# Kernel optimization log

Hardware: AMD Instinct MI355X
Metric: run time of the kernel (lower is better)

The kernel has to match this reference:

```python
import jax, jax.numpy as jnp
import numpy as np

N = 4096        # nodes == batch_size (GFN operates on dense N x N adjacency)
E = 65536       # edges per view (avg degree 16)
IN = 512        # per-view input feature dim
HV = [128, 64]  # per-view GCN dims
HM = [64, 64]   # fused-graph GCN dims
VIEWS = 3


def setup_inputs() -> dict:
    key = jax.random.key(0)
    ks = iter(jax.random.split(key, 64))

    def xavier(shape):
        lim = float(np.sqrt(6.0 / (shape[0] + shape[1])))
        return jax.random.uniform(next(ks), shape, minval=-lim, maxval=lim, dtype=jnp.float32)

    inp = {}
    for v in range(VIEWS):
        inp[f"x{v}"] = jax.random.normal(next(ks), (N, IN), dtype=jnp.float32)
        inp[f"src{v}"] = jax.random.randint(next(ks), (E,), 0, N, dtype=jnp.int32)
        inp[f"dst{v}"] = jax.random.randint(next(ks), (E,), 0, N, dtype=jnp.int32)
        inp[f"Wv{v}0"] = xavier((IN, HV[0]))
        inp[f"bv{v}0"] = jnp.zeros((HV[0],), jnp.float32)
        inp[f"Wv{v}1"] = xavier((HV[0], HV[1]))
        inp[f"bv{v}1"] = jnp.zeros((HV[1],), jnp.float32)
        inp[f"Wf{v}"] = xavier((HV[1], HV[1]))  # FeatureFusion weight
    # GFN: Linear(N -> N/2) -> ReLU -> Linear(N/2 -> N)
    inp["Wg1"] = xavier((N, N // 2)); inp["bg1"] = jnp.zeros((N // 2,), jnp.float32)
    inp["Wg2"] = xavier((N // 2, N)); inp["bg2"] = jnp.zeros((N,), jnp.float32)
    # fused-graph GCN layers
    inp["Wm0"] = xavier((HV[1], HM[0])); inp["bm0"] = jnp.zeros((HM[0],), jnp.float32)
    inp["Wm1"] = xavier((HM[0], HM[1])); inp["bm1"] = jnp.zeros((HM[1],), jnp.float32)
    return inp


def _deg_norms(src, dst):
    # DGL GraphConv norm='both': scale by out-deg(src)^-1/2 and in-deg(dst)^-1/2, degrees clamped to >=1
    ones = jnp.ones(src.shape[0], jnp.float32)
    dout = jnp.maximum(jax.ops.segment_sum(ones, src, num_segments=N), 1.0)
    din = jnp.maximum(jax.ops.segment_sum(ones, dst, num_segments=N), 1.0)
    return dout ** -0.5, din ** -0.5


def _gconv(x, W, b, src, dst, do_isqrt, di_isqrt, act):
    h = (x * do_isqrt[:, None]) @ W            # [N, out] (W commutes with row scaling)
    agg = jax.ops.segment_sum(h[src], dst, num_segments=N)
    h = agg * di_isqrt[:, None] + b
    return act(h)


def reference(x0, x1, x2, src0, dst0, src1, dst1, src2, dst2,
              Wv00, bv00, Wv01, bv01, Wv10, bv10, Wv11, bv11, Wv20, bv20, Wv21, bv21,
              Wf0, Wf1, Wf2, Wg1, bg1, Wg2, bg2, Wm0, bm0, Wm1, bm1):
    ident = lambda t: t
    xs = [x0, x1, x2]
    edges = [(src0, dst0), (src1, dst1), (src2, dst2)]
    Wv = [(Wv00, bv00, Wv01, bv01), (Wv10, bv10, Wv11, bv11), (Wv20, bv20, Wv21, bv21)]
    Wf = [Wf0, Wf1, Wf2]

    # per-view GCN stacks (relu on first layer, identity on last)
    feats = []
    for v in range(VIEWS):
        src, dst = edges[v]
        do_i, di_i = _deg_norms(src, dst)
        W0, b0, W1, b1 = Wv[v]
        f = _gconv(xs[v], W0, b0, src, dst, do_i, di_i, jax.nn.relu)
        f = _gconv(f, W1, b1, src, dst, do_i, di_i, ident)
        feats.append(f)

    # FeatureFusion (dropout omitted for determinism): sum(f @ Wf), softmax over features, relu
    z = feats[0] @ Wf[0] + feats[1] @ Wf[1] + feats[2] @ Wf[2]
    z = jax.nn.relu(jax.nn.softmax(z, axis=1))

    # consensus graph: sum of per-view dense adjacencies -> GFN -> clamp -> round(+0.1)
    adj = jnp.zeros((N, N), jnp.float32)
    for src, dst in edges:
        adj = adj + jnp.zeros((N, N), jnp.float32).at[src, dst].set(1.0)
    fused = jax.nn.relu(adj @ Wg1 + bg1) @ Wg2 + bg2
    fused = jnp.round(jnp.clip(fused, 0.0, 1.0) + 0.1)
    adj_r = fused

    # rebuild binary graph (went through numpy in original -> stop_gradient), symmetrize, add self-loops
    sym = jax.lax.stop_gradient(fused)
    sym = sym + sym.T
    A = jnp.maximum((sym > 0).astype(jnp.float32), jnp.eye(N, dtype=jnp.float32))
    deg = A.sum(axis=1)
    dn = deg ** -0.5

    # fused-graph GCN layers (dense normalized SpMM form since A is already dense)
    h = z
    h = jax.nn.relu(((A @ (h * dn[:, None])) * dn[:, None]) @ Wm0 + bm0)
    h = ((A @ (h * dn[:, None])) * dn[:, None]) @ Wm1 + bm1

    # InnerProductDecoder with identity activation; all `views` entries of adj_rec are identical
    adj_rec = h @ h.T
    return (adj_r, adj_rec, h)
```

## Files before the change

### kernel.cpp

```cpp
#include <hip/hip_runtime.h>
#include <math.h>

#define NNODES 4096
#define NEDGES 65536

typedef short bf16x8 __attribute__((ext_vector_type(8)));
typedef short short4v __attribute__((ext_vector_type(4)));
typedef float f32x4 __attribute__((ext_vector_type(4)));

struct Ptr3  { const float* p[3]; };
struct Ptr3i { const int*   p[3]; };
struct Ptr3h { const short* p[3]; };

__device__ __forceinline__ short f2bf(float f) {
    unsigned u = __builtin_bit_cast(unsigned, f);
    unsigned r = (u + 0x7FFFu + ((u >> 16) & 1u)) >> 16;
    return (short)r;
}

__device__ __forceinline__ void gload_lds16(const void* g, void* l) {
    __builtin_amdgcn_global_load_lds(
        (const __attribute__((address_space(1))) unsigned*)g,
        (__attribute__((address_space(3))) unsigned*)l, 16, 0, 0);
}

template<int BN, int ACT>
__global__ __launch_bounds__(512, 1)
void g8_k(const short* __restrict__ A, const short* __restrict__ Bt,
          const float* __restrict__ bias, void* __restrict__ Cout,
          unsigned char* __restrict__ Pout, int M, int Nn, int K, int lda, int ldb)
{
    constexpr int SLOT_SH = 16384 + BN * 64;
    constexpr int WN = (BN == 256) ? 4 : 2;
    constexpr int TM = (BN == 256) ? 128 : 64;
    constexpr int MF = TM / 32;
    __shared__ short lds[2 * SLOT_SH];

    const int tid = threadIdx.x;
    const int lane = tid & 63;
    const int wave = tid >> 6;
    const int wm = wave / WN, wn = wave % WN;
    const int gx = gridDim.x, nwg = gx * gridDim.y;
    int w = blockIdx.y * gx + blockIdx.x;
    const int q8 = nwg >> 3;
    w = (w & 7) * q8 + (w >> 3);
    const int bm0 = (w / gx) * 256, bn0 = (w % gx) * BN;

    const int NT = K >> 6;

    f32x4 acc[2 * MF][4] = {};
    bf16x8 aF[MF][2];
    bf16x8 bF[2][2][2];

    auto stageQ = [&](int t, int sel) {
        if (sel < 0 || t >= NT) return;
        const int k0 = t << 6;
        short* L = lds + (t & 1) * SLOT_SH;
        const int rowq = tid >> 3;
        const int slot8 = tid & 7;
        const int woff = wave * 512;
#pragma unroll
        for (int u = 0; u < 2; ++u) {
            int strip, isB;
            if (sel == 0)      { strip = u * 2;     isB = 0; }
            else if (sel == 1) { strip = u * 2 + 1; isB = 0; }
            else if (sel == 2) { strip = u;         isB = 1; }
            else               { strip = u + 2;     isB = 1; }
            const int grow = strip * 64 + rowq;
            const int scol = (slot8 ^ (grow & 7)) << 3;
            if (!isB)
                gload_lds16(A + (size_t)(bm0 + grow) * lda + k0 + scol,
                            L + strip * 4096 + woff);
            else
                gload_lds16(Bt + (size_t)(bn0 + grow) * ldb + k0 + scol,
                            L + 16384 + strip * 4096 + woff);
        }
    };

#define PHASE(Q, TCUR, STAGET, SSEL, VM)                                              \
    {                                                                                 \
        constexpr int mh_ = (Q) >> 1, nh_ = (Q) & 1;                                  \
        const short* As_ = lds + ((TCUR) & 1) * SLOT_SH;                              \
        const short* Bs_ = As_ + 16384;                                               \
        if constexpr ((Q) == 0 || (Q) == 2) {                                         \
            _Pragma("unroll") for (int kk = 0; kk < 2; ++kk) {                        \
                const int h_ = kk * 4 + (lane >> 4);                                  \
                _Pragma("unroll") for (int i = 0; i < MF; ++i) {                      \
                    int r_ = wm * TM + mh_ * (TM / 2) + i * 16 + (lane & 15);         \
                    aF[i][kk] = *(const bf16x8*)(As_ + r_ * 64 + ((h_ ^ (r_ & 7)) << 3)); \
                }                                                                     \
            }                                                                         \
        }                                                                             \
        if constexpr ((Q) == 0 || (Q) == 1) {                                         \
            _Pragma("unroll") for (int kk = 0; kk < 2; ++kk) {                        \
                const int h_ = kk * 4 + (lane >> 4);                                  \
                _Pragma("unroll") for (int j = 0; j < 2; ++j) {                       \
                    int r_ = wn * 64 + nh_ * 32 + j * 16 + (lane & 15);               \
                    bF[nh_][j][kk] = *(const bf16x8*)(Bs_ + r_ * 64 + ((h_ ^ (r_ & 7)) << 3)); \
                }                                                                     \
            }                                                                         \
        }                                                                             \
        stageQ(STAGET, SSEL);                                                         \
        __builtin_amdgcn_s_barrier();                                                 \
        __builtin_amdgcn_s_setprio(1);                                                \
        _Pragma("unroll") for (int kk = 0; kk < 2; ++kk)                              \
            _Pragma("unroll") for (int i = 0; i < MF; ++i)                            \
                _Pragma("unroll") for (int j = 0; j < 2; ++j)                         \
                    acc[mh_ * MF + i][nh_ * 2 + j] =                                  \
                        __builtin_amdgcn_mfma_f32_16x16x32_bf16(                      \
                            aF[i][kk], bF[nh_][j][kk], acc[mh_ * MF + i][nh_ * 2 + j], 0, 0, 0); \
        __builtin_amdgcn_s_setprio(0);                                                \
        if ((VM) == 2)      { asm volatile("s_waitcnt vmcnt(2)" ::: "memory"); }      \
        else if ((VM) == 0) { asm volatile("s_waitcnt vmcnt(0)" ::: "memory"); }      \
        __builtin_amdgcn_sched_barrier(0);                                            \
        __builtin_amdgcn_s_barrier();                                                 \
    }

    stageQ(0, 0); stageQ(0, 1); stageQ(0, 2);
    if constexpr (BN == 256) stageQ(0, 3);
    stageQ(1, 0);
    asm volatile("s_waitcnt vmcnt(2)" ::: "memory");
    __builtin_amdgcn_sched_barrier(0);
    __builtin_amdgcn_s_barrier();

    constexpr int SB = (BN == 256) ? 3 : -1;
    for (int it = 0; it < NT / 2; ++it) {
        const int t0 = 2 * it, t1 = t0 + 1;
        PHASE(0, t0, t1, 1, -1);
        PHASE(1, t0, t1, 2, -1);
        PHASE(2, t0, t1, SB, -1);
        { int vm_ = (t0 + 2 < NT) ? 2 : 0; PHASE(3, t0, t0 + 2, 0, vm_); }
        PHASE(0, t1, t0 + 2, 1, -1);
        PHASE(1, t1, t0 + 2, 2, -1);
        PHASE(2, t1, t0 + 2, SB, -1);
        { int vm_ = (t0 + 2 < NT) ? 2 : -1; PHASE(3, t1, t0 + 3, 0, vm_); }
    }
#undef PHASE

    const int cr = (lane >> 4) * 4;
    const int cc = lane & 15;
#pragma unroll
    for (int im = 0; im < 2 * MF; ++im) {
#pragma unroll
        for (int jn = 0; jn < 4; ++jn) {
            int col = bn0 + wn * 64 + (jn >> 1) * 32 + (jn & 1) * 16 + cc;
            float bv = bias ? bias[col] : 0.f;
#pragma unroll
            for (int q2 = 0; q2 < 4; ++q2) {
                int row = bm0 + wm * TM + (im / MF) * (TM / 2) + (im % MF) * 16 + cr + q2;
                float v = acc[im][jn][q2] + bv;
                if constexpr (ACT == 1) {
                    v = fmaxf(v, 0.f);
                    ((short*)Cout)[(size_t)row * Nn + col] = f2bf(v);
                } else if constexpr (ACT == 2) {
                    v = rintf(fminf(fmaxf(v, 0.f), 1.f) + 0.1f);
                    ((float*)Cout)[(size_t)row * Nn + col] = v;
                    Pout[(size_t)row * Nn + col] = (unsigned char)(v > 0.5f);
                } else {
                    ((float*)Cout)[(size_t)row * Nn + col] = v;
                }
            }
        }
    }
}

template<int ACT>
__global__ __launch_bounds__(512, 1)
void gemm256_k(const short* __restrict__ A, const short* __restrict__ Bt,
               const float* __restrict__ bias, void* __restrict__ Cout,
               unsigned char* __restrict__ Pout, int M, int Nn, int K)
{
    __shared__ short lds_s[3 * 24576];
    const int tid = threadIdx.x;
    const int lane = tid & 63;
    const int gx = gridDim.x, nwg = gx * gridDim.y;
    int w = blockIdx.y * gx + blockIdx.x;
    const int q = nwg >> 3;
    w = (w & 7) * q + (w >> 3);
    const int bm0 = (w / gx) * 256, bn0 = (w % gx) * 128;
    const int wmr = ((tid >> 6) >> 1) * 64;
    const int wnr = ((tid >> 6) & 1) * 64;
    const int NT = K >> 6;

    auto stage = [&](int kt, int slot) {
        const int k0 = kt << 6;
        char* base = (char*)(lds_s + slot * 24576);
        char* wbase = base + (tid >> 6) * 1024;
#pragma unroll
        for (int r = 0; r < 4; ++r) {
            int o = r * 8192 + tid * 16;
            int row = o >> 7;
            int sl = (o >> 4) & 7;
            gload_lds16(A + ((size_t)(bm0 + row) * K + k0 + ((sl ^ (row & 7)) << 3)),
                        wbase + r * 8192);
        }
#pragma unroll
        for (int r = 0; r < 2; ++r) {
            int o = r * 8192 + tid * 16;
            int row = o >> 7;
            int sl = (o >> 4) & 7;
            gload_lds16(Bt + ((size_t)(bn0 + row) * K + k0 + ((sl ^ (row & 7)) << 3)),
                        base + 32768 + r * 8192 + (tid >> 6) * 1024);
        }
    };

    f32x4 acc[4][4] = {};
    stage(0, 0);
    if (NT > 1) stage(1, 1);

    for (int kt = 0; kt < NT; ++kt) {
        if (kt < NT - 1) { asm volatile("s_waitcnt vmcnt(6)" ::: "memory"); }
        else             { asm volatile("s_waitcnt vmcnt(0)" ::: "memory"); }
        __builtin_amdgcn_s_barrier();
        if (kt + 2 < NT) stage(kt + 2, (kt + 2) % 3);

        const short* As = lds_s + (kt % 3) * 24576;
        const short* Bs = As + 16384;
        __builtin_amdgcn_s_setprio(1);
#pragma unroll
        for (int kk = 0; kk < 2; ++kk) {
            bf16x8 a[4], b[4];
            const int khalf = kk * 4 + (lane >> 4);
#pragma unroll
            for (int i = 0; i < 4; ++i) {
                int r = wmr + i * 16 + (lane & 15);
                a[i] = *(const bf16x8*)(As + r * 64 + ((khalf ^ (r & 7)) << 3));
            }
#pragma unroll
            for (int j = 0; j < 4; ++j) {
                int r = wnr + j * 16 + (lane & 15);
                b[j] = *(const bf16x8*)(Bs + r * 64 + ((khalf ^ (r & 7)) << 3));
            }
#pragma unroll
            for (int i = 0; i < 4; ++i)
#pragma unroll
                for (int j = 0; j < 4; ++j)
                    acc[i][j] = __builtin_amdgcn_mfma_f32_16x16x32_bf16(a[i], b[j], acc[i][j], 0, 0, 0);
        }
        __builtin_amdgcn_s_setprio(0);
        asm volatile("s_waitcnt lgkmcnt(0)" ::: "memory");
    }

    const int cr = (lane >> 4) * 4;
    const int cc = lane & 15;
#pragma unroll
    for (int i = 0; i < 4; ++i)
#pragma unroll
        for (int j = 0; j < 4; ++j) {
            int col = bn0 + wnr + j * 16 + cc;
#pragma unroll
            for (int q2 = 0; q2 < 4; ++q2) {
                int row = bm0 + wmr + i * 16 + cr + q2;
                ((float*)Cout)[(size_t)row * Nn + col] = acc[i][j][q2];
            }
        }
}

__global__ __launch_bounds__(256)
void mfma_gemm_b_k(const short* __restrict__ Aall, Ptr3h Btv, float* __restrict__ Call,
                   int M, int Nn, int K)
{
    __shared__ short As[64 * 64];
    __shared__ short Bs[64 * 64];
    const int z = blockIdx.z;
    const short* A = Aall + (size_t)z * M * K;
    const short* Bt = Btv.p[z];
    float* C = Call + (size_t)z * M * Nn;
    const int tid = threadIdx.x;
    const int lane = tid & 63, wave = tid >> 6;
    const int bm0 = blockIdx.y * 64, bn0 = blockIdx.x * 64;
    const int wr = (wave >> 1) * 32, wc = (wave & 1) * 32;

    f32x4 acc[2][2] = {};

    for (int k0 = 0; k0 < K; k0 += 64) {
        for (int c = wave; c < 8; c += 4) {
            int o = c * 1024 + lane * 16;
            int row = o >> 7;
            int sl = (o >> 4) & 7;
            int ss = sl ^ (row & 7);
            gload_lds16(A + ((size_t)(bm0 + row) * K + k0 + ss * 8), As + c * 512);
            gload_lds16(Bt + ((size_t)(bn0 + row) * K + k0 + ss * 8), Bs + c * 512);
        }
        __syncthreads();
#pragma unroll
        for (int kk = 0; kk < 2; ++kk) {
            bf16x8 a[2], b[2];
            const int khalf = kk * 4 + (lane >> 4);
#pragma unroll
            for (int i = 0; i < 2; ++i) {
                int r = wr + i * 16 + (lane & 15);
                a[i] = *(const bf16x8*)(As + r * 64 + ((khalf ^ (r & 7)) << 3));
            }
#pragma unroll
            for (int j = 0; j < 2; ++j) {
                int r = wc + j * 16 + (lane & 15);
                b[j] = *(const bf16x8*)(Bs + r * 64 + ((khalf ^ (r & 7)) << 3));
            }
#pragma unroll
            for (int i = 0; i < 2; ++i)
#pragma unroll
                for (int j = 0; j < 2; ++j)
                    acc[i][j] = __builtin_amdgcn_mfma_f32_16x16x32_bf16(a[i], b[j], acc[i][j], 0, 0, 0);
        }
        __syncthreads();
    }

    const int cr = (lane >> 4) * 4;
    const int cc = lane & 15;
#pragma unroll
    for (int i = 0; i < 2; ++i)
#pragma unroll
        for (int j = 0; j < 2; ++j)
#pragma unroll
            for (int q = 0; q < 4; ++q) {
                int row = bm0 + wr + i * 16 + cr + q;
                int col = bn0 + wc + j * 16 + cc;
                C[(size_t)row * Nn + col] = acc[i][j][q];
            }
}

__global__ __launch_bounds__(256)
void spmm_mfma_k(const short* __restrict__ A2b, const short* __restrict__ XsT,
                 float* __restrict__ part)
{
    __shared__ short As[64 * 64];
    __shared__ short Bs[128 * 64];
    const int tid = threadIdx.x;
    const int lane = tid & 63, wave = tid >> 6;
    const int kc = blockIdx.x, m0 = blockIdx.y * 64;
    const int wr = (wave >> 1) * 32, wc = (wave & 1) * 32;
    const int woff = wave * 512;

    f32x4 acc[2][2] = {};

    for (int k0 = kc * 512; k0 < kc * 512 + 512; k0 += 64) {
#pragma unroll
        for (int r = 0; r < 2; ++r) {
            int o = r * 4096 + tid * 16;
            int row = o >> 7;
            int sl = (o >> 4) & 7;
            gload_lds16(A2b + ((size_t)(m0 + row) * 4096 + k0 + ((sl ^ (row & 7)) << 3)),
                        As + r * 2048 + woff);
        }
#pragma unroll
        for (int r = 0; r < 4; ++r) {
            int o = r * 4096 + tid * 16;
            int row = o >> 7;
            int sl = (o >> 4) & 7;
            gload_lds16(XsT + ((size_t)row * 4096 + k0 + ((sl ^ (row & 7)) << 3)),
                        Bs + r * 2048 + woff);
        }
        __syncthreads();
#pragma unroll
        for (int kk = 0; kk < 2; ++kk) {
            const int h = kk * 4 + (lane >> 4);
            bf16x8 a[2], bh[2], bl[2];
#pragma unroll
            for (int i = 0; i < 2; ++i) {
                int r = wr + i * 16 + (lane & 15);
                a[i] = *(const bf16x8*)(As + r * 64 + ((h ^ (r & 7)) << 3));
            }
#pragma unroll
            for (int j = 0; j < 2; ++j) {
                int r = wc + j * 16 + (lane & 15);
                bh[j] = *(const bf16x8*)(Bs + r * 64 + ((h ^ (r & 7)) << 3));
                int r2 = r + 64;
                bl[j] = *(const bf16x8*)(Bs + r2 * 64 + ((h ^ (r2 & 7)) << 3));
            }
#pragma unroll
            for (int i = 0; i < 2; ++i)
#pragma unroll
                for (int j = 0; j < 2; ++j) {
                    acc[i][j] = __builtin_amdgcn_mfma_f32_16x16x32_bf16(a[i], bh[j], acc[i][j], 0, 0, 0);
                    acc[i][j] = __builtin_amdgcn_mfma_f32_16x16x32_bf16(a[i], bl[j], acc[i][j], 0, 0, 0);
                }
        }
        __syncthreads();
    }

    const int cr = (lane >> 4) * 4;
    const int cc = lane & 15;
#pragma unroll
    for (int i = 0; i < 2; ++i)
#pragma unroll
        for (int j = 0; j < 2; ++j)
#pragma unroll
            for (int q = 0; q < 4; ++q)
                part[((size_t)kc * NNODES + m0 + wr + i * 16 + cr + q) * 64 + wc + j * 16 + cc]
                    = acc[i][j][q];
}

__global__ void xsT_k(const float* __restrict__ X, const int* __restrict__ degA,
                      short* __restrict__ XsT)
{
    const int n = blockIdx.y;
    const int k = blockIdx.x * 256 + threadIdx.x;
    float v = X[(size_t)k * 64 + n] * (1.0f / sqrtf((float)degA[k]));
    short hi = f2bf(v);
    float hif = __builtin_bit_cast(float, ((unsigned)(unsigned short)hi) << 16);
    short lo = f2bf(v - hif);
    XsT[(size_t)n * 4096 + k] = hi;
    XsT[(size_t)(64 + n) * 4096 + k] = lo;
}

__global__ void a2b_k(const unsigned* __restrict__ A8w, short* __restrict__ A2b, int words)
{
    int t = blockIdx.x * 256 + threadIdx.x;
    if (t < words) {
        unsigned w = A8w[t];
        short4v o;
#pragma unroll
        for (int j = 0; j < 4; ++j) o[j] = ((w >> (8 * j)) & 1u) ? (short)0x3F80 : (short)0;
        *(short4v*)(A2b + (size_t)t * 4) = o;
    }
}

__global__ void f32_to_bf16T_k(const float* __restrict__ src, short* __restrict__ dstT,
                               int R, int C)
{
    __shared__ float t[64][65];
    const int br = blockIdx.y * 64, bc = blockIdx.x * 64;
    for (int idx = threadIdx.x; idx < 64 * 64; idx += 256) {
        int r = idx >> 6, c = idx & 63;
        t[r][c] = src[(size_t)(br + r) * C + bc + c];
    }
    __syncthreads();
    for (int idx = threadIdx.x; idx < 64 * 64; idx += 256) {
        int c = idx >> 6, r = idx & 63;
        dstT[(size_t)(bc + c) * R + br + r] = f2bf(t[r][c]);
    }
}

__global__ void mask_to_bf16_k(const unsigned* __restrict__ mask, short* __restrict__ adj,
                               int words)
{
    int t = blockIdx.x * 256 + threadIdx.x;
    if (t < words) {
        unsigned w = mask[t];
        short4v o;
        o.x = f2bf((float)__popc(w & 0x7u));
        o.y = f2bf((float)__popc(w & 0x700u));
        o.z = f2bf((float)__popc(w & 0x70000u));
        o.w = f2bf((float)__popc(w & 0x7000000u));
        *(short4v*)(adj + (size_t)t * 4) = o;
    }
}

__global__ void xsplit_k(Ptr3 xv, const float* __restrict__ isq, short* __restrict__ xe)
{
    const int z = blockIdx.y;
    int t = blockIdx.x * 256 + threadIdx.x;
    int n = t >> 9, k = t & 511;
    float a = xv.p[z][(size_t)n * 512 + k] * isq[2 * z * NNODES + n];
    short hi = f2bf(a);
    float hif = __builtin_bit_cast(float, ((unsigned)(unsigned short)hi) << 16);
    short lo = f2bf(a - hif);
    short* row = xe + (size_t)z * NNODES * 1536 + (size_t)n * 1536;
    row[k] = hi; row[512 + k] = hi; row[1024 + k] = lo;
}

__global__ void wsplitT_k(Ptr3 Wv, short* __restrict__ out, int K, int Nn)
{
    const int z = blockIdx.y;
    int t = blockIdx.x * 256 + threadIdx.x;
    if (t >= K * Nn) return;
    int k = t / Nn, n = t % Nn;
    float w = Wv.p[z][(size_t)k * Nn + n];
    short hi = f2bf(w);
    float hif = __builtin_bit_cast(float, ((unsigned)(unsigned short)hi) << 16);
    short lo = f2bf(w - hif);
    short* row = out + (size_t)z * Nn * 3 * K + (size_t)n * 3 * K;
    row[k] = hi; row[K + k] = lo; row[2 * K + k] = hi;
}

template<int RELU>
__global__ __launch_bounds__(256)
void redgemm_k(const float* __restrict__ part, const int* __restrict__ degA,
               const float* __restrict__ Wm, const float* __restrict__ bias,
               float* __restrict__ out, short* __restrict__ Ae, short* __restrict__ Be)
{
    __shared__ float Ws[64 * 64];
    const int tid = threadIdx.x;
    for (int i = tid; i < 4096; i += 256) Ws[i] = Wm[i];
    __syncthreads();
    const int lane = tid & 63, wave = tid >> 6;
    const float bv = bias[lane];
    for (int rr = 0; rr < 16; ++rr) {
        int row = blockIdx.x * 64 + wave * 16 + rr;
        float s = 0.f;
#pragma unroll
        for (int p = 0; p < 8; ++p) s += part[((size_t)p * NNODES + row) * 64 + lane];
        s *= 1.0f / sqrtf((float)degA[row]);
        float acc = bv;
#pragma unroll
        for (int k = 0; k < 64; ++k)
            acc = fmaf(__shfl(s, k), Ws[k * 64 + lane], acc);
        if (RELU) acc = fmaxf(acc, 0.f);
        out[(size_t)row * 64 + lane] = acc;
        if (Ae) {
            short hi = f2bf(acc);
            float hif = __builtin_bit_cast(float, ((unsigned)(unsigned short)hi) << 16);
            short lo = f2bf(acc - hif);
            size_t ro = (size_t)row * 192;
            Ae[ro + lane] = hi; Ae[ro + 64 + lane] = hi; Ae[ro + 128 + lane] = lo;
            Be[ro + lane] = hi; Be[ro + 64 + lane] = lo; Be[ro + 128 + lane] = hi;
        }
    }
}

__global__ void edge_k(Ptr3i src, Ptr3i dst, unsigned* __restrict__ mask, int* __restrict__ degs)
{
    int e = blockIdx.x * 256 + threadIdx.x;
    int z = blockIdx.y;
    if (e < NEDGES) {
        int s = src.p[z][e], d = dst.p[z][e];
        unsigned c = (unsigned)s * (unsigned)NNODES + (unsigned)d;
        atomicOr(&mask[c >> 2], 1u << ((c & 3u) * 8u + (unsigned)z));
        atomicAdd(&degs[2 * z * NNODES + s], 1);
        atomicAdd(&degs[(2 * z + 1) * NNODES + d], 1);
    }
}

__global__ void deg_norm_k(const int* __restrict__ degs, float* __restrict__ isq, int n)
{
    int t = blockIdx.x * 256 + threadIdx.x;
    if (t < n) isq[t] = 1.0f / sqrtf(fmaxf((float)degs[t], 1.0f));
}

__global__ __launch_bounds__(1024)
void scan_k(const int* __restrict__ degs, int* __restrict__ rowptr, int* __restrict__ cursor)
{
    const int z = blockIdx.x;
    const int* din = degs + (2 * z + 1) * NNODES;
    __shared__ int sm[1024];
    const int t = threadIdx.x;
    int v0 = din[t * 4], v1 = din[t * 4 + 1], v2 = din[t * 4 + 2], v3 = din[t * 4 + 3];
    int c1 = v0 + v1, c2 = c1 + v2, s = c2 + v3;
    sm[t] = s;
    __syncthreads();
    for (int off = 1; off < 1024; off <<= 1) {
        int add = (t >= off) ? sm[t - off] : 0;
        __syncthreads();
        sm[t] += add;
        __syncthreads();
    }
    int base = sm[t] - s;
    int* rp = rowptr + z * NNODES;
    int* cu = cursor + z * NNODES;
    rp[t * 4] = base;          cu[t * 4] = base;
    rp[t * 4 + 1] = base + v0; cu[t * 4 + 1] = base + v0;
    rp[t * 4 + 2] = base + c1; cu[t * 4 + 2] = base + c1;
    rp[t * 4 + 3] = base + c2; cu[t * 4 + 3] = base + c2;
}

__global__ void fill_k(Ptr3i src, Ptr3i dst, int* __restrict__ cursor, int* __restrict__ eidx)
{
    int e = blockIdx.x * 256 + threadIdx.x;
    int z = blockIdx.y;
    if (e < NEDGES) {
        int d = dst.p[z][e];
        int pos = atomicAdd(&cursor[z * NNODES + d], 1);
        eidx[(size_t)z * NEDGES + pos] = src.p[z][e];
    }
}

template<int F, int ACT, int MODE>
__global__ void gather_k(const float* __restrict__ Hpre, const int* __restrict__ eidx,
                         const int* __restrict__ rowptr, const int* __restrict__ degs,
                         const float* __restrict__ isq, Ptr3 bias, short* __restrict__ Sout)
{
    const int z = blockIdx.y;
    const int tid = threadIdx.x;
    const int node = blockIdx.x * (256 / F) + tid / F;
    const int f = tid % F;
    const float* H = Hpre + (size_t)z * NNODES * F;
    const int base = rowptr[z * NNODES + node];
    const int cnt = degs[(2 * z + 1) * NNODES + node];
    const int* ei = eidx + (size_t)z * NEDGES + base;
    float s = 0.f;
    for (int i = 0; i < cnt; ++i) s += H[(size_t)ei[i] * F + f];
    float v = s * isq[(2 * z + 1) * NNODES + node] + bias.p[z][f];
    if (ACT) v = fmaxf(v, 0.f);
    if (MODE == 1) v *= isq[2 * z * NNODES + node];
    short hi = f2bf(v);
    float hif = __builtin_bit_cast(float, ((unsigned)(unsigned short)hi) << 16);
    short lo = f2bf(v - hif);
    short* row = Sout + (size_t)z * NNODES * 3 * F + (size_t)node * 3 * F;
    row[f] = hi; row[F + f] = hi; row[2 * F + f] = lo;
}

__global__ void softsum_k(const float* __restrict__ zp, float* __restrict__ z)
{
    int row = blockIdx.x * 4 + (threadIdx.x >> 6);
    int f = threadIdx.x & 63;
    size_t i = (size_t)row * 64 + f;
    float v = zp[i] + zp[i + (size_t)NNODES * 64] + zp[i + (size_t)2 * NNODES * 64];
    float m = v;
#pragma unroll
    for (int off = 32; off >= 1; off >>= 1) m = fmaxf(m, __shfl_xor(m, off));
    float e = expf(v - m);
    float s = e;
#pragma unroll
    for (int off = 32; off >= 1; off >>= 1) s += __shfl_xor(s, off);
    z[i] = e / s;
}

__global__ __launch_bounds__(256)
void build_A2_k(const unsigned char* __restrict__ P, unsigned char* __restrict__ A8,
                int* __restrict__ degA)
{
    __shared__ unsigned Ts[64][20];
    const int bi = blockIdx.y * 64, bj = blockIdx.x * 64;
    const int tid = threadIdx.x;
    const int r = tid >> 2, seg = tid & 3;
    uint4 tv = *(const uint4*)(P + (size_t)(bj + r) * NNODES + bi + seg * 16);
    Ts[r][seg * 4 + 0] = tv.x; Ts[r][seg * 4 + 1] = tv.y;
    Ts[r][seg * 4 + 2] = tv.z; Ts[r][seg * 4 + 3] = tv.w;
    __syncthreads();
    uint4 dv = *(const uint4*)(P + (size_t)(bi + r) * NNODES + bj + seg * 16);
    unsigned dw[4] = {dv.x, dv.y, dv.z, dv.w};
    const unsigned char* Tb = (const unsigned char*)Ts;
    unsigned ow[4];
    int psum = 0;
#pragma unroll
    for (int w = 0; w < 4; ++w) {
        unsigned o = 0;
#pragma unroll
        for (int b = 0; b < 4; ++b) {
            int j = seg * 16 + w * 4 + b;
            unsigned a = (dw[w] >> (8 * b)) & 1u;
            unsigned tr = Tb[j * 80 + r] & 1u;
            unsigned on = a | tr | (unsigned)((bi + r) == (bj + j));
            o |= on << (8 * b);
            psum += (int)on;
        }
        ow[w] = o;
    }
    uint4 o4; o4.x = ow[0]; o4.y = ow[1]; o4.z = ow[2]; o4.w = ow[3];
    *(uint4*)(A8 + (size_t)(bi + r) * NNODES + bj + seg * 16) = o4;
    psum += __shfl_xor(psum, 1);
    psum += __shfl_xor(psum, 2);
    if (seg == 0) atomicAdd(&degA[bi + r], psum);
}

extern "C" void kernel_launch(void* const* d_in, const int* in_sizes, int n_in,
                              void* d_out, int out_size, void* d_ws, size_t ws_size,
                              hipStream_t stream)
{
    const int N = NNODES, E = NEDGES;
    const size_t MB = 1024 * 1024;

    const float* x[3]; const int* src[3]; const int* dst[3];
    const float *Wv0[3], *bv0[3], *Wv1[3], *bv1[3], *Wf[3];
    for (int v = 0; v < 3; ++v) {
        const int b = v * 8;
        x[v]   = (const float*)d_in[b + 0];
        src[v] = (const int*)  d_in[b + 1];
        dst[v] = (const int*)  d_in[b + 2];
        Wv0[v] = (const float*)d_in[b + 3];
        bv0[v] = (const float*)d_in[b + 4];
        Wv1[v] = (const float*)d_in[b + 5];
        bv1[v] = (const float*)d_in[b + 6];
        Wf[v]  = (const float*)d_in[b + 7];
    }
    const float* Wg1 = (const float*)d_in[24];
    const float* bg1 = (const float*)d_in[25];
    const float* Wg2 = (const float*)d_in[26];
    const float* bg2 = (const float*)d_in[27];
    const float* Wm0 = (const float*)d_in[28];
    const float* bm0 = (const float*)d_in[29];
    const float* Wm1 = (const float*)d_in[30];
    const float* bm1 = (const float*)d_in[31];

    float* out_adjr = (float*)d_out;
    float* out_rec  = out_adjr + (size_t)N * N;
    float* out_h    = out_rec + (size_t)N * N;

    char* oa = (char*)out_adjr;
    short* AdjB = (short*)oa;
    float* hv1  = (float*)(oa + 32 * MB);
    short* Ae2  = (short*)(oa + 38 * MB);
    short* Ae3  = (short*)(oa + 47 * MB);
    float* hv2  = (float*)(oa + 52 * MB);
    float* zp   = (float*)(oa + 56 * MB);

    char* orc = (char*)out_rec;
    short* xe   = (short*)orc;
    short* H1b  = (short*)orc;
    unsigned char* P = (unsigned char*)(orc + 16 * MB);
    short* Wg1T = (short*)(orc + 16 * MB);
    short* Wg2T = (short*)(orc + 32 * MB);
    short* A2b  = (short*)orc;
    float* part = (float*)(orc + 48 * MB);

    char* p = (char*)d_ws;
    unsigned* mask = (unsigned*)p;
    unsigned char* A8 = (unsigned char*)p;
    short* AeF = (short*)p;
    short* BeF = AeF + (size_t)N * 192;
    p += (size_t)N * N;
    int* degs = (int*)p;     p += (size_t)6 * N * 4;
    float* isq = (float*)p;  p += (size_t)6 * N * 4;
    int* rowptr = (int*)p;   p += (size_t)3 * N * 4;
    int* cursor = (int*)p;   p += (size_t)3 * N * 4;
    int* eidx = (int*)p;     p += (size_t)3 * E * 4;
    int* degA = (int*)p;     p += (size_t)N * 4;
    float* zbuf = (float*)p; p += (size_t)N * 64 * 4;
    float* h1m = (float*)p;  p += (size_t)N * 64 * 4;
    short* XsT = (short*)p;  p += (size_t)128 * N * 2;
    short* Wv0T = (short*)p; p += (size_t)3 * 128 * 1536 * 2;
    short* Wv1T = (short*)p; p += (size_t)3 * 64 * 384 * 2;
    short* WfT  = (short*)p; p += (size_t)3 * 64 * 192 * 2;

    Ptr3i srcP, dstP;
    for (int v = 0; v < 3; ++v) { srcP.p[v] = src[v]; dstP.p[v] = dst[v]; }

    hipMemsetAsync(mask, 0, (size_t)N * N, stream);
    hipMemsetAsync(degs, 0, (size_t)6 * N * 4, stream);

    edge_k<<<dim3((E + 255) / 256, 3), 256, 0, stream>>>(srcP, dstP, mask, degs);
    deg_norm_k<<<(6 * N + 255) / 256, 256, 0, stream>>>(degs, isq, 6 * N);
    scan_k<<<3, 1024, 0, stream>>>(degs, rowptr, cursor);
    fill_k<<<dim3((E + 255) / 256, 3), 256, 0, stream>>>(srcP, dstP, cursor, eidx);

    Ptr3 xP; for (int v = 0; v < 3; ++v) xP.p[v] = x[v];
    xsplit_k<<<dim3(N * 512 / 256, 3), 256, 0, stream>>>(xP, isq, xe);
    Ptr3 wP;
    for (int v = 0; v < 3; ++v) wP.p[v] = Wv0[v];
    wsplitT_k<<<dim3(512 * 128 / 256, 3), 256, 0, stream>>>(wP, Wv0T, 512, 128);
    for (int v = 0; v < 3; ++v) wP.p[v] = Wv1[v];
    wsplitT_k<<<dim3(128 * 64 / 256, 3), 256, 0, stream>>>(wP, Wv1T, 128, 64);
    for (int v = 0; v < 3; ++v) wP.p[v] = Wf[v];
    wsplitT_k<<<dim3(64 * 64 / 256, 3), 256, 0, stream>>>(wP, WfT, 64, 64);

    Ptr3h BtP; Ptr3 biasP;
    for (int v = 0; v < 3; ++v) BtP.p[v] = Wv0T + (size_t)v * 128 * 1536;
    mfma_gemm_b_k<<<dim3(2, N / 64, 3), 256, 0, stream>>>(xe, BtP, hv1, N, 128, 1536);
    for (int v = 0; v < 3; ++v) biasP.p[v] = bv0[v];
    gather_k<128, 1, 1><<<dim3(N / 2, 3), 256, 0, stream>>>(hv1, eidx, rowptr, degs, isq, biasP, Ae2);
    for (int v = 0; v < 3; ++v) BtP.p[v] = Wv1T + (size_t)v * 64 * 384;
    mfma_gemm_b_k<<<dim3(1, N / 64, 3), 256, 0, stream>>>(Ae2, BtP, hv2, N, 64, 384);
    for (int v = 0; v < 3; ++v) biasP.p[v] = bv1[v];
    gather_k<64, 0, 2><<<dim3(N / 4, 3), 256, 0, stream>>>(hv2, eidx, rowptr, degs, isq, biasP, Ae3);
    for (int v = 0; v < 3; ++v) BtP.p[v] = WfT + (size_t)v * 64 * 192;
    mfma_gemm_b_k<<<dim3(1, N / 64, 3), 256, 0, stream>>>(Ae3, BtP, zp, N, 64, 192);
    softsum_k<<<N / 4, 256, 0, stream>>>(zp, zbuf);

    mask_to_bf16_k<<<(N * N / 4 + 255) / 256, 256, 0, stream>>>(mask, AdjB, N * N / 4);
    f32_to_bf16T_k<<<dim3(2048 / 64, 4096 / 64), 256, 0, stream>>>(Wg1, Wg1T, 4096, 2048);

    g8_k<128, 1><<<dim3(2048 / 128, 4096 / 256), 512, 0, stream>>>(
        AdjB, Wg1T, bg1, H1b, nullptr, 4096, 2048, 4096, 4096, 4096);

    f32_to_bf16T_k<<<dim3(4096 / 64, 2048 / 64), 256, 0, stream>>>(Wg2, Wg2T, 2048, 4096);

    g8_k<256, 2><<<dim3(4096 / 256, 4096 / 256), 512, 0, stream>>>(
        H1b, Wg2T, bg2, out_adjr, P, 4096, 4096, 2048, 2048, 2048);

    hipMemsetAsync(degA, 0, (size_t)N * 4, stream);
    build_A2_k<<<dim3(N / 64, N / 64), 256, 0, stream>>>(P, A8, degA);

    a2b_k<<<(N * N / 4 + 255) / 256, 256, 0, stream>>>((const unsigned*)A8, A2b, N * N / 4);
    xsT_k<<<dim3(16, 64), 256, 0, stream>>>(zbuf, degA, XsT);
    spmm_mfma_k<<<dim3(8, N / 64), 256, 0, stream>>>(A2b, XsT, part);
    redgemm_k<1><<<64, 256, 0, stream>>>(part, degA, Wm0, bm0, h1m, nullptr, nullptr);
    xsT_k<<<dim3(16, 64), 256, 0, stream>>>(h1m, degA, XsT);
    spmm_mfma_k<<<dim3(8, N / 64), 256, 0, stream>>>(A2b, XsT, part);
    redgemm_k<0><<<64, 256, 0, stream>>>(part, degA, Wm1, bm1, out_h, AeF, BeF);

    gemm256_k<0><<<dim3(4096 / 128, 4096 / 256), 512, 0, stream>>>(
        AeF, BeF, nullptr, out_rec, nullptr, 4096, 4096, 192);
}
```

Before: 528.4 us.

## Unify GEMMs on a triple-buffered 256x128 kernel and widen redgemm grid

Replaces the templated double-buffered g8_k (two tile widths, four phases per k-tile) with one 256x128-tile kernel. It uses a three-slot LDS ring and two half-phases per k-tile that interleave staging with MFMA. The GFN second GEMM now uses 128-wide tiles, doubling its grid, and the decoder GEMM reuses this kernel instead of the separate gemm256_k. redgemm_k now runs 256 blocks of 16 rows instead of 64 blocks of 64 rows, to spread the small reduction across more CUs. The narrower tile re-reads A more often for the 4096x4096 GEMM, and deeper buffering uses more LDS.

```diff
diff --git a/kernel.cpp b/kernel.cpp
--- a/kernel.cpp
+++ b/kernel.cpp
@@ -24,131 +24,126 @@
         (__attribute__((address_space(3))) unsigned*)l, 16, 0, 0);
 }
 
-template<int BN, int ACT>
+template<int ACT>
 __global__ __launch_bounds__(512, 1)
 void g8_k(const short* __restrict__ A, const short* __restrict__ Bt,
           const float* __restrict__ bias, void* __restrict__ Cout,
           unsigned char* __restrict__ Pout, int M, int Nn, int K, int lda, int ldb)
 {
-    constexpr int SLOT_SH = 16384 + BN * 64;
-    constexpr int WN = (BN == 256) ? 4 : 2;
-    constexpr int TM = (BN == 256) ? 128 : 64;
-    constexpr int MF = TM / 32;
-    __shared__ short lds[2 * SLOT_SH];
-
+    constexpr int SLOT = 24576;
+    __shared__ short lds[3 * SLOT];
     const int tid = threadIdx.x;
     const int lane = tid & 63;
     const int wave = tid >> 6;
-    const int wm = wave / WN, wn = wave % WN;
+    const int wm = wave >> 1, wn = wave & 1;
     const int gx = gridDim.x, nwg = gx * gridDim.y;
     int w = blockIdx.y * gx + blockIdx.x;
     const int q8 = nwg >> 3;
     w = (w & 7) * q8 + (w >> 3);
-    const int bm0 = (w / gx) * 256, bn0 = (w % gx) * BN;
-
+    const int bm0 = (w / gx) * 256, bn0 = (w % gx) * 128;
     const int NT = K >> 6;
 
-    f32x4 acc[2 * MF][4] = {};
-    bf16x8 aF[MF][2];
-    bf16x8 bF[2][2][2];
-
-    auto stageQ = [&](int t, int sel) {
-        if (sel < 0 || t >= NT) return;
+    auto stageR = [&](int t, int part) {
+        if (t >= NT) return;
         const int k0 = t << 6;
-        short* L = lds + (t & 1) * SLOT_SH;
-        const int rowq = tid >> 3;
-        const int slot8 = tid & 7;
-        const int woff = wave * 512;
-#pragma unroll
-        for (int u = 0; u < 2; ++u) {
-            int strip, isB;
-            if (sel == 0)      { strip = u * 2;     isB = 0; }
-            else if (sel == 1) { strip = u * 2 + 1; isB = 0; }
-            else if (sel == 2) { strip = u;         isB = 1; }
-            else               { strip = u + 2;     isB = 1; }
-            const int grow = strip * 64 + rowq;
-            const int scol = (slot8 ^ (grow & 7)) << 3;
-            if (!isB)
-                gload_lds16(A + (size_t)(bm0 + grow) * lda + k0 + scol,
-                            L + strip * 4096 + woff);
-            else
-                gload_lds16(Bt + (size_t)(bn0 + grow) * ldb + k0 + scol,
-                            L + 16384 + strip * 4096 + woff);
+        char* base = (char*)(lds + (t % 3) * SLOT);
+#pragma unroll
+        for (int r = 0; r < 2; ++r) {
+            int ra = part * 2 + r;
+            int o = ra * 8192 + tid * 16;
+            int row = o >> 7;
+            int sl = (o >> 4) & 7;
+            gload_lds16(A + ((size_t)(bm0 + row) * lda + k0 + ((sl ^ (row & 7)) << 3)),
+                        base + ra * 8192 + wave * 1024);
+        }
+        {
+            int o = part * 8192 + tid * 16;
+            int row = o >> 7;
+            int sl = (o >> 4) & 7;
+            gload_lds16(Bt + ((size_t)(bn0 + row) * ldb + k0 + ((sl ^ (row & 7)) << 3)),
+                        base + 32768 + part * 8192 + wave * 1024);
         }
     };
 
-#define PHASE(Q, TCUR, STAGET, SSEL, VM)                                              \
-    {                                                                                 \
-        constexpr int mh_ = (Q) >> 1, nh_ = (Q) & 1;                                  \
-        const short* As_ = lds + ((TCUR) & 1) * SLOT_SH;                              \
-        const short* Bs_ = As_ + 16384;                                               \
-        if constexpr ((Q) == 0 || (Q) == 2) {                                         \
-            _Pragma("unroll") for (int kk = 0; kk < 2; ++kk) {                        \
-                const int h_ = kk * 4 + (lane >> 4);                                  \
-                _Pragma("unroll") for (int i = 0; i < MF; ++i) {                      \
-                    int r_ = wm * TM + mh_ * (TM / 2) + i * 16 + (lane & 15);         \
-                    aF[i][kk] = *(const bf16x8*)(As_ + r_ * 64 + ((h_ ^ (r_ & 7)) << 3)); \
-                }                                                                     \
-            }                                                                         \
-        }                                                                             \
-        if constexpr ((Q) == 0 || (Q) == 1) {                                         \
-            _Pragma("unroll") for (int kk = 0; kk < 2; ++kk) {                        \
-                const int h_ = kk * 4 + (lane >> 4);                                  \
-                _Pragma("unroll") for (int j = 0; j < 2; ++j) {                       \
-                    int r_ = wn * 64 + nh_ * 32 + j * 16 + (lane & 15);               \
-                    bF[nh_][j][kk] = *(const bf16x8*)(Bs_ + r_ * 64 + ((h_ ^ (r_ & 7)) << 3)); \
-                }                                                                     \
-            }                                                                         \
-        }                                                                             \
-        stageQ(STAGET, SSEL);                                                         \
-        __builtin_amdgcn_s_barrier();                                                 \
-        __builtin_amdgcn_s_setprio(1);                                                \
-        _Pragma("unroll") for (int kk = 0; kk < 2; ++kk)                              \
-            _Pragma("unroll") for (int i = 0; i < MF; ++i)                            \
-                _Pragma("unroll") for (int j = 0; j < 2; ++j)                         \
-                    acc[mh_ * MF + i][nh_ * 2 + j] =                                  \
-                        __builtin_amdgcn_mfma_f32_16x16x32_bf16(                      \
-                            aF[i][kk], bF[nh_][j][kk], acc[mh_ * MF + i][nh_ * 2 + j], 0, 0, 0); \
-        __builtin_amdgcn_s_setprio(0);                                                \
-        if ((VM) == 2)      { asm volatile("s_waitcnt vmcnt(2)" ::: "memory"); }      \
-        else if ((VM) == 0) { asm volatile("s_waitcnt vmcnt(0)" ::: "memory"); }      \
-        __builtin_amdgcn_sched_barrier(0);                                            \
-        __builtin_amdgcn_s_barrier();                                                 \
-    }
-
-    stageQ(0, 0); stageQ(0, 1); stageQ(0, 2);
-    if constexpr (BN == 256) stageQ(0, 3);
-    stageQ(1, 0);
-    asm volatile("s_waitcnt vmcnt(2)" ::: "memory");
+    f32x4 acc[4][4] = {};
+    bf16x8 bF[4][2];
+
+    stageR(0, 0); stageR(0, 1);
+    stageR(1, 0); stageR(1, 1);
+    asm volatile("s_waitcnt vmcnt(6)" ::: "memory");
     __builtin_amdgcn_sched_barrier(0);
     __builtin_amdgcn_s_barrier();
 
-    constexpr int SB = (BN == 256) ? 3 : -1;
-    for (int it = 0; it < NT / 2; ++it) {
-        const int t0 = 2 * it, t1 = t0 + 1;
-        PHASE(0, t0, t1, 1, -1);
-        PHASE(1, t0, t1, 2, -1);
-        PHASE(2, t0, t1, SB, -1);
-        { int vm_ = (t0 + 2 < NT) ? 2 : 0; PHASE(3, t0, t0 + 2, 0, vm_); }
-        PHASE(0, t1, t0 + 2, 1, -1);
-        PHASE(1, t1, t0 + 2, 2, -1);
-        PHASE(2, t1, t0 + 2, SB, -1);
-        { int vm_ = (t0 + 2 < NT) ? 2 : -1; PHASE(3, t1, t0 + 3, 0, vm_); }
-    }
-#undef PHASE
+    for (int t = 0; t < NT; ++t) {
+        const short* As_ = lds + (t % 3) * SLOT;
+        const short* Bs_ = As_ + 16384;
+        bf16x8 aF[2][2];
+#pragma unroll
+        for (int kk = 0; kk < 2; ++kk) {
+            const int h = kk * 4 + (lane >> 4);
+#pragma unroll
+            for (int j = 0; j < 4; ++j) {
+                int r = wn * 64 + j * 16 + (lane & 15);
+                bF[j][kk] = *(const bf16x8*)(Bs_ + r * 64 + ((h ^ (r & 7)) << 3));
+            }
+#pragma unroll
+            for (int i = 0; i < 2; ++i) {
+                int r = wm * 64 + i * 16 + (lane & 15);
+                aF[i][kk] = *(const bf16x8*)(As_ + r * 64 + ((h ^ (r & 7)) << 3));
+            }
+        }
+        stageR(t + 2, 0);
+        __builtin_amdgcn_s_barrier();
+        __builtin_amdgcn_s_setprio(1);
+#pragma unroll
+        for (int kk = 0; kk < 2; ++kk)
+#pragma unroll
+            for (int i = 0; i < 2; ++i)
+#pragma unroll
+                for (int j = 0; j < 4; ++j)
+                    acc[i][j] = __builtin_amdgcn_mfma_f32_16x16x32_bf16(
+                        aF[i][kk], bF[j][kk], acc[i][j], 0, 0, 0);
+        __builtin_amdgcn_s_setprio(0);
+        __builtin_amdgcn_s_barrier();
+#pragma unroll
+        for (int kk = 0; kk < 2; ++kk) {
+            const int h = kk * 4 + (lane >> 4);
+#pragma unroll
+            for (int i = 0; i < 2; ++i) {
+                int r = wm * 64 + 32 + i * 16 + (lane & 15);
+                aF[i][kk] = *(const bf16x8*)(As_ + r * 64 + ((h ^ (r & 7)) << 3));
+            }
+        }
+        stageR(t + 2, 1);
+        __builtin_amdgcn_s_barrier();
+        __builtin_amdgcn_s_setprio(1);
+#pragma unroll
+        for (int kk = 0; kk < 2; ++kk)
+#pragma unroll
+            for (int i = 0; i < 2; ++i)
+#pragma unroll
+                for (int j = 0; j < 4; ++j)
+                    acc[2 + i][j] = __builtin_amdgcn_mfma_f32_16x16x32_bf16(
+                        aF[i][kk], bF[j][kk], acc[2 + i][j], 0, 0, 0);
+        __builtin_amdgcn_s_setprio(0);
+        if (t + 2 < NT) { asm volatile("s_waitcnt vmcnt(6)" ::: "memory"); }
+        else            { asm volatile("s_waitcnt vmcnt(0)" ::: "memory"); }
+        __builtin_amdgcn_sched_barrier(0);
+        __builtin_amdgcn_s_barrier();
+    }
 
     const int cr = (lane >> 4) * 4;
     const int cc = lane & 15;
 #pragma unroll
-    for (int im = 0; im < 2 * MF; ++im) {
-#pragma unroll
-        for (int jn = 0; jn < 4; ++jn) {
-            int col = bn0 + wn * 64 + (jn >> 1) * 32 + (jn & 1) * 16 + cc;
+    for (int im = 0; im < 4; ++im) {
+#pragma unroll
+        for (int j = 0; j < 4; ++j) {
+            int col = bn0 + wn * 64 + j * 16 + cc;
             float bv = bias ? bias[col] : 0.f;
 #pragma unroll
             for (int q2 = 0; q2 < 4; ++q2) {
-                int row = bm0 + wm * TM + (im / MF) * (TM / 2) + (im % MF) * 16 + cr + q2;
-                float v = acc[im][jn][q2] + bv;
+                int row = bm0 + wm * 64 + (im >> 1) * 32 + (im & 1) * 16 + cr + q2;
+                float v = acc[im][j][q2] + bv;
                 if constexpr (ACT == 1) {
                     v = fmaxf(v, 0.f);
                     ((short*)Cout)[(size_t)row * Nn + col] = f2bf(v);
@@ -164,98 +159,6 @@
     }
 }
 
-template<int ACT>
-__global__ __launch_bounds__(512, 1)
-void gemm256_k(const short* __restrict__ A, const short* __restrict__ Bt,
-               const float* __restrict__ bias, void* __restrict__ Cout,
-               unsigned char* __restrict__ Pout, int M, int Nn, int K)
-{
-    __shared__ short lds_s[3 * 24576];
-    const int tid = threadIdx.x;
-    const int lane = tid & 63;
-    const int gx = gridDim.x, nwg = gx * gridDim.y;
-    int w = blockIdx.y * gx + blockIdx.x;
-    const int q = nwg >> 3;
-    w = (w & 7) * q + (w >> 3);
-    const int bm0 = (w / gx) * 256, bn0 = (w % gx) * 128;
-    const int wmr = ((tid >> 6) >> 1) * 64;
-    const int wnr = ((tid >> 6) & 1) * 64;
-    const int NT = K >> 6;
-
-    auto stage = [&](int kt, int slot) {
-        const int k0 = kt << 6;
-        char* base = (char*)(lds_s + slot * 24576);
-        char* wbase = base + (tid >> 6) * 1024;
-#pragma unroll
-        for (int r = 0; r < 4; ++r) {
-            int o = r * 8192 + tid * 16;
-            int row = o >> 7;
-            int sl = (o >> 4) & 7;
-            gload_lds16(A + ((size_t)(bm0 + row) * K + k0 + ((sl ^ (row & 7)) << 3)),
-                        wbase + r * 8192);
-        }
-#pragma unroll
-        for (int r = 0; r < 2; ++r) {
-            int o = r * 8192 + tid * 16;
-            int row = o >> 7;
-            int sl = (o >> 4) & 7;
-            gload_lds16(Bt + ((size_t)(bn0 + row) * K + k0 + ((sl ^ (row & 7)) << 3)),
-                        base + 32768 + r * 8192 + (tid >> 6) * 1024);
-        }
-    };
-
-    f32x4 acc[4][4] = {};
-    stage(0, 0);
-    if (NT > 1) stage(1, 1);
-
-    for (int kt = 0; kt < NT; ++kt) {
-        if (kt < NT - 1) { asm volatile("s_waitcnt vmcnt(6)" ::: "memory"); }
-        else             { asm volatile("s_waitcnt vmcnt(0)" ::: "memory"); }
-        __builtin_amdgcn_s_barrier();
-        if (kt + 2 < NT) stage(kt + 2, (kt + 2) % 3);
-
-        const short* As = lds_s + (kt % 3) * 24576;
-        const short* Bs = As + 16384;
-        __builtin_amdgcn_s_setprio(1);
-#pragma unroll
-        for (int kk = 0; kk < 2; ++kk) {
-            bf16x8 a[4], b[4];
-            const int khalf = kk * 4 + (lane >> 4);
-#pragma unroll
-            for (int i = 0; i < 4; ++i) {
-                int r = wmr + i * 16 + (lane & 15);
-                a[i] = *(const bf16x8*)(As + r * 64 + ((khalf ^ (r & 7)) << 3));
-            }
-#pragma unroll
-            for (int j = 0; j < 4; ++j) {
-                int r = wnr + j * 16 + (lane & 15);
-                b[j] = *(const bf16x8*)(Bs + r * 64 + ((khalf ^ (r & 7)) << 3));
-            }
-#pragma unroll
-            for (int i = 0; i < 4; ++i)
-#pragma unroll
-                for (int j = 0; j < 4; ++j)
-                    acc[i][j] = __builtin_amdgcn_mfma_f32_16x16x32_bf16(a[i], b[j], acc[i][j], 0, 0, 0);
-        }
-        __builtin_amdgcn_s_setprio(0);
-        asm volatile("s_waitcnt lgkmcnt(0)" ::: "memory");
-    }
-
-    const int cr = (lane >> 4) * 4;
-    const int cc = lane & 15;
-#pragma unroll
-    for (int i = 0; i < 4; ++i)
-#pragma unroll
-        for (int j = 0; j < 4; ++j) {
-            int col = bn0 + wnr + j * 16 + cc;
-#pragma unroll
-            for (int q2 = 0; q2 < 4; ++q2) {
-                int row = bm0 + wmr + i * 16 + cr + q2;
-                ((float*)Cout)[(size_t)row * Nn + col] = acc[i][j][q2];
-            }
-        }
-}
-
 __global__ __launch_bounds__(256)
 void mfma_gemm_b_k(const short* __restrict__ Aall, Ptr3h Btv, float* __restrict__ Call,
                    int M, int Nn, int K)
@@ -486,8 +389,8 @@
     __syncthreads();
     const int lane = tid & 63, wave = tid >> 6;
     const float bv = bias[lane];
-    for (int rr = 0; rr < 16; ++rr) {
-        int row = blockIdx.x * 64 + wave * 16 + rr;
+    for (int rr = 0; rr < 4; ++rr) {
+        int row = blockIdx.x * 16 + wave * 4 + rr;
         float s = 0.f;
 #pragma unroll
         for (int p = 0; p < 8; ++p) s += part[((size_t)p * NNODES + row) * 64 + lane];
@@ -750,12 +653,12 @@
     mask_to_bf16_k<<<(N * N / 4 + 255) / 256, 256, 0, stream>>>(mask, AdjB, N * N / 4);
     f32_to_bf16T_k<<<dim3(2048 / 64, 4096 / 64), 256, 0, stream>>>(Wg1, Wg1T, 4096, 2048);
 
-    g8_k<128, 1><<<dim3(2048 / 128, 4096 / 256), 512, 0, stream>>>(
+    g8_k<1><<<dim3(2048 / 128, 4096 / 256), 512, 0, stream>>>(
         AdjB, Wg1T, bg1, H1b, nullptr, 4096, 2048, 4096, 4096, 4096);
 
     f32_to_bf16T_k<<<dim3(4096 / 64, 2048 / 64), 256, 0, stream>>>(Wg2, Wg2T, 2048, 4096);
 
-    g8_k<256, 2><<<dim3(4096 / 256, 4096 / 256), 512, 0, stream>>>(
+    g8_k<2><<<dim3(4096 / 128, 4096 / 256), 512, 0, stream>>>(
         H1b, Wg2T, bg2, out_adjr, P, 4096, 4096, 2048, 2048, 2048);
 
     hipMemsetAsync(degA, 0, (size_t)N * 4, stream);
@@ -764,11 +667,11 @@
     a2b_k<<<(N * N / 4 + 255) / 256, 256, 0, stream>>>((const unsigned*)A8, A2b, N * N / 4);
     xsT_k<<<dim3(16, 64), 256, 0, stream>>>(zbuf, degA, XsT);
     spmm_mfma_k<<<dim3(8, N / 64), 256, 0, stream>>>(A2b, XsT, part);
-    redgemm_k<1><<<64, 256, 0, stream>>>(part, degA, Wm0, bm0, h1m, nullptr, nullptr);
+    redgemm_k<1><<<256, 256, 0, stream>>>(part, degA, Wm0, bm0, h1m, nullptr, nullptr);
     xsT_k<<<dim3(16, 64), 256, 0, stream>>>(h1m, degA, XsT);
     spmm_mfma_k<<<dim3(8, N / 64), 256, 0, stream>>>(A2b, XsT, part);
-    redgemm_k<0><<<64, 256, 0, stream>>>(part, degA, Wm1, bm1, out_h, AeF, BeF);
-
-    gemm256_k<0><<<dim3(4096 / 128, 4096 / 256), 512, 0, stream>>>(
-        AeF, BeF, nullptr, out_rec, nullptr, 4096, 4096, 192);
-}
+    redgemm_k<0><<<256, 256, 0, stream>>>(part, degA, Wm1, bm1, out_h, AeF, BeF);
+
+    g8_k<0><<<dim3(4096 / 128, 4096 / 256), 512, 0, stream>>>(
+        AeF, BeF, nullptr, out_rec, nullptr, 4096, 4096, 192, 192, 192);
+}
```

Result: faster. 455.1 us (-13.9%).
